# Performance work log

Hardware: AMD Instinct MI355X
Metric: run time of the kernel (lower is better)

The kernel has to match this reference:

```python
import jax, jax.numpy as jnp
import numpy as np

N_TYPES = 4  # global / and / or / leaf node types (indep_weights)


def gcn_layer(x, W_stack, b, edge_src, edge_dst, edge_w, labels, num_nodes):
    # Per-node-type dense projection: compute all 4 projections, then select by label.
    # all4: [4, N, out]
    all4 = jnp.einsum('nd,kdo->kno', x, W_stack)
    support = jnp.take_along_axis(all4, labels[None, :, None].astype(jnp.int32), axis=0)[0]  # [N, out]
    # Sparse adjacency propagation: out[dst] += w * support[src]  (torch.spmm equivalent)
    msgs = support[edge_src] * edge_w[:, None]  # [E, out]
    agg = jax.ops.segment_sum(msgs, edge_dst, num_segments=num_nodes)
    return agg + b


def setup_inputs() -> dict:
    key = jax.random.key(0)
    ks = jax.random.split(key, 12)
    N, E = 50000, 1600000
    nfeat, nhid, nclass = 256, 256, 64
    x = jax.random.normal(ks[0], (N, nfeat), dtype=jnp.float32)
    edge_src = jax.random.randint(ks[1], (E,), 0, N, dtype=jnp.int32)
    edge_dst = jax.random.randint(ks[2], (E,), 0, N, dtype=jnp.int32)
    edge_w = jax.random.uniform(ks[3], (E,), dtype=jnp.float32)
    labels = jax.random.randint(ks[4], (N,), 0, N_TYPES, dtype=jnp.int32)
    def winit(k, fi, fo):
        s = 1.0 / np.sqrt(fo)
        return jax.random.uniform(k, (N_TYPES, fi, fo), minval=-s, maxval=s, dtype=jnp.float32)
    def binit(k, fo):
        s = 1.0 / np.sqrt(fo)
        return jax.random.uniform(k, (fo,), minval=-s, maxval=s, dtype=jnp.float32)
    return {
        'x': x, 'edge_src': edge_src, 'edge_dst': edge_dst, 'edge_w': edge_w, 'labels': labels,
        'W1': winit(ks[5], nfeat, nhid), 'b1': binit(ks[6], nhid),
        'W2': winit(ks[7], nhid, nhid), 'b2': binit(ks[8], nhid),
        'W3': winit(ks[9], nhid, nclass), 'b3': binit(ks[10], nclass),
    }


def reference(x, edge_src, edge_dst, edge_w, labels, W1, b1, W2, b2, W3, b3):
    N = x.shape[0]
    h = jax.nn.relu(gcn_layer(x, W1, b1, edge_src, edge_dst, edge_w, labels, N))
    # F.dropout with p=0 (module default) is identity
    h = jax.nn.relu(gcn_layer(h, W2, b2, edge_src, edge_dst, edge_w, labels, N))
    out = gcn_layer(h, W3, b3, edge_src, edge_dst, edge_w, labels, N)
    return out
```

## Files before the change

### kernel.cpp

```cpp
#include <hip/hip_runtime.h>
#include <hip/hip_bf16.h>

#define NT 4
#define FEAT 256
#define OUT3 64

typedef __bf16 bf16x8 __attribute__((ext_vector_type(8)));
typedef float  f32x4  __attribute__((ext_vector_type(4)));

__device__ inline unsigned int f2bf_bits(float f) {
    __hip_bfloat16 h = __float2bfloat16(f);
    unsigned short u;
    __builtin_memcpy(&u, &h, 2);
    return (unsigned int)u;
}
__device__ inline float bfl(unsigned int u) { return __uint_as_float(u << 16); }
__device__ inline float bfh(unsigned int u) { return __uint_as_float(u & 0xffff0000u); }
__device__ __host__ inline int nat_of(int p) {
    int lo = p & 63;
    return (p & ~63) | (((lo & 3) << 4) | (lo >> 2));
}

__global__ __launch_bounds__(512) void pass_a(const int* __restrict__ dst,
                                              const int* __restrict__ labels,
                                              int* __restrict__ bcnt, int* __restrict__ lc,
                                              int E, int N) {
    __shared__ int h[256];
    __shared__ int lh[NT];
    int tid = threadIdx.x;
    if (tid < 256) h[tid] = 0;
    if (tid < NT) lh[tid] = 0;
    __syncthreads();
    int base = blockIdx.x * 4096;
#pragma unroll
    for (int k = 0; k < 8; ++k) {
        int e = base + k * 512 + tid;
        if (e < E) atomicAdd(&h[((unsigned)dst[e]) >> 8], 1);
    }
#pragma unroll
    for (int k = 0; k < 8; ++k) {
        int i = base + k * 512 + tid;
        if (i < N) atomicAdd(&lh[labels[i]], 1);
    }
    __syncthreads();
    if (tid < 256) { int v = h[tid]; if (v) atomicAdd(&bcnt[tid], v); }
    if (tid < NT) { int v = lh[tid]; if (v) atomicAdd(&lc[tid], v); }
}

__global__ __launch_bounds__(256) void scan_master(
    const int* __restrict__ bcnt, const int* __restrict__ lc,
    int* __restrict__ boff, int* __restrict__ gcur, int* __restrict__ rowoff,
    int* __restrict__ lstart, int NB, int N, int E) {
    __shared__ int s[256];
    int tid = threadIdx.x;
    int own = (tid < NB) ? bcnt[tid] : 0;
    s[tid] = own;
    __syncthreads();
    for (int d = 1; d < 256; d <<= 1) {
        int v = (tid >= d) ? s[tid - d] : 0;
        __syncthreads();
        s[tid] += v;
        __syncthreads();
    }
    int excl = s[tid] - own;
    if (tid < NB) { boff[tid] = excl; gcur[tid] = excl; }
    if (tid == 0) {
        boff[NB] = E; rowoff[N] = E;
        int run = 0;
        for (int l = 0; l < NT; ++l) {
            lstart[l] = run;
            run += (lc[l] + 63) & ~63;
        }
    }
}

__global__ void scatter_nodes(const int* __restrict__ labels, const int* __restrict__ lstart,
                              int* __restrict__ lcur, int* __restrict__ iperm, int N) {
    int n = blockIdx.x * 256 + threadIdx.x;
    int lab = (n < N) ? labels[n] : -1;
    int lane = threadIdx.x & 63;
    for (int l = 0; l < NT; ++l) {
        unsigned long long m = __ballot(lab == l);
        if (m == 0ull) continue;
        int leader = __builtin_ctzll(m);
        int base = 0;
        if (lane == leader) base = atomicAdd(&lcur[l], (int)__popcll(m));
        base = __shfl(base, leader, 64);
        if (lab == l) {
            int prefix = (int)__popcll(m & ((1ull << lane) - 1ull));
            iperm[n] = lstart[l] + base + prefix;
        }
    }
}

__global__ __launch_bounds__(512) void scatter_edges(
    const int* __restrict__ src, const int* __restrict__ dst, const float* __restrict__ w,
    const int* __restrict__ iperm, int* __restrict__ gcur, uint2* __restrict__ earr, int E) {
    __shared__ int h[256];
    __shared__ int basearr[256];
    int tid = threadIdx.x;
    if (tid < 256) h[tid] = 0;
    __syncthreads();
    int base = blockIdx.x * 4096;
    int b[8], rank[8], px[8]; float wv[8];
#pragma unroll
    for (int k = 0; k < 8; ++k) {
        int e = base + k * 512 + tid;
        if (e < E) {
            int d = dst[e];
            b[k] = ((unsigned)d) >> 8;
            px[k] = iperm[src[e]] | ((d & 255) << 16);
            wv[k] = w[e];
            rank[k] = atomicAdd(&h[b[k]], 1);
        } else b[k] = -1;
    }
    __syncthreads();
    if (tid < 256) { int c = h[tid]; basearr[tid] = c ? atomicAdd(&gcur[tid], c) : 0; }
    __syncthreads();
#pragma unroll
    for (int k = 0; k < 8; ++k) {
        if (b[k] >= 0) {
            int pos = basearr[b[k]] + rank[k];
            earr[pos] = make_uint2((unsigned)px[k], __float_as_uint(wv[k]));
        }
    }
}

__global__ __launch_bounds__(1024) void bucket_sort(
    const uint2* __restrict__ earr, const int* __restrict__ boff,
    int* __restrict__ rowoff, unsigned int* __restrict__ edata, int N) {
    int b = blockIdx.x;
    int s = boff[b], e = boff[b + 1];
    __shared__ int cnt[256], off[256];
    int tid = threadIdx.x;
    if (tid < 256) cnt[tid] = 0;
    __syncthreads();
    for (int i = s + tid; i < e; i += 1024) atomicAdd(&cnt[(earr[i].x >> 16) & 255], 1);
    __syncthreads();
    if (tid < 256) off[tid] = cnt[tid];
    __syncthreads();
    for (int d = 1; d < 256; d <<= 1) {
        int v = 0;
        if (tid < 256 && tid >= d) v = off[tid - d];
        __syncthreads();
        if (tid < 256) off[tid] += v;
        __syncthreads();
    }
    if (tid < 256) {
        int excl = off[tid] - cnt[tid];
        int node = b * 256 + tid;
        if (node < N) rowoff[node] = s + excl;
        off[tid] = excl;
    }
    __syncthreads();
    for (int i = s + tid; i < e; i += 1024) {
        uint2 r = earr[i];
        int d = (r.x >> 16) & 255;
        int k = atomicAdd(&off[d], 1);
        edata[s + k] = (f2bf_bits(__uint_as_float(r.y)) << 16) | (r.x & 0xffff);
    }
}

__global__ void cast_x(const float* __restrict__ x, const int* __restrict__ iperm,
                       unsigned short* __restrict__ actLo, unsigned short* __restrict__ actHi,
                       int total4) {
    int i = blockIdx.x * 256 + threadIdx.x;
    if (i < total4) {
        float4 v = ((const float4*)x)[i];
        unsigned int lo = f2bf_bits(v.x) | (f2bf_bits(v.y) << 16);
        unsigned int hi = f2bf_bits(v.z) | (f2bf_bits(v.w) << 16);
        int slot = iperm[i >> 6];
        unsigned short* dst = ((i & 63) >= 32) ? actHi : actLo;
        ((uint2*)dst)[(size_t)slot * 32 + (i & 31)] = make_uint2(lo, hi);
    }
}

__global__ void cast_w_all(const float* __restrict__ W1, const float* __restrict__ W2,
                           const float* __restrict__ W3, const float* __restrict__ b1,
                           const float* __restrict__ b2,
                           unsigned short* __restrict__ W1b, unsigned short* __restrict__ W2b,
                           unsigned short* __restrict__ W3b, float* __restrict__ biasPerm) {
    const int S = NT * FEAT * FEAT;
    const int S3 = NT * FEAT * OUT3;
    int idx = blockIdx.x * 256 + threadIdx.x;
    if (idx < 2 * S + S3) {
        const float* W; unsigned short* D; int OUTF; int t; bool remap;
        if (idx < S)          { W = W1; D = W1b; OUTF = FEAT; t = idx;         remap = false; }
        else if (idx < 2 * S) { W = W2; D = W2b; OUTF = FEAT; t = idx - S;     remap = true; }
        else                  { W = W3; D = W3b; OUTF = OUT3; t = idx - 2 * S; remap = true; }
        int n = t % OUTF;
        int r = t / OUTF;
        int j = r & 7, q = (r >> 3) & 3, k0 = (r >> 5) & 7, lab = r >> 8;
        int k_slot = k0 * 32 + q * 8 + j;
        int k_src = remap ? nat_of(k_slot) : k_slot;
        float f = W[((size_t)(lab * FEAT + k_src)) * OUTF + n];
        D[(((size_t)lab * 8 + k0) * OUTF + n) * 32 + q * 8 + j] = (unsigned short)f2bf_bits(f);
    } else {
        int p = idx - (2 * S + S3);
        if (p < 256) biasPerm[p] = b1[nat_of(p)];
        else if (p < 512) biasPerm[p] = b2[nat_of(p - 256)];
    }
}

__global__ __launch_bounds__(256) void proj256_kernel(
    const unsigned short* __restrict__ actLo, const unsigned short* __restrict__ actHi,
    const unsigned short* __restrict__ Wswz, const int* __restrict__ lstart,
    unsigned short* __restrict__ supLo, unsigned short* __restrict__ supHi) {
    int warp = threadIdx.x >> 6;
    int lane = threadIdx.x & 63;
    int m0 = blockIdx.x * 64;
    int lab = (m0 >= lstart[1]) + (m0 >= lstart[2]) + (m0 >= lstart[3]);
    int q = lane >> 4, c = lane & 15;
    int n0 = warp * 64;

    const unsigned short* aLo = actLo + (size_t)(m0 + c) * 128 + q * 8;
    const unsigned short* aHi = actHi + (size_t)(m0 + c) * 128 + q * 8;
    const unsigned short* bb = Wswz + (size_t)lab * FEAT * 256 + (size_t)(n0 + c) * 32 + q * 8;

    f32x4 acc[4][4] = {};
#pragma unroll
    for (int k0 = 0; k0 < 8; ++k0) {
        const unsigned short* abase = (k0 < 4) ? aLo : aHi;
        int koff = (k0 & 3) * 32;
        bf16x8 a[4];
#pragma unroll
        for (int t = 0; t < 4; ++t) a[t] = *(const bf16x8*)(abase + (size_t)t * 2048 + koff);
        const unsigned short* bk = bb + (size_t)k0 * 32 * 256;
#pragma unroll
        for (int u = 0; u < 4; ++u) {
            bf16x8 bfrag = *(const bf16x8*)(bk + u * 512);
#pragma unroll
            for (int t = 0; t < 4; ++t)
                acc[t][u] = __builtin_amdgcn_mfma_f32_16x16x32_bf16(a[t], bfrag, acc[t][u], 0, 0, 0);
        }
    }
    uint2* ov = (uint2*)((n0 >= 128) ? supHi : supLo);
    int cix = ((n0 & 64) >> 2) + c;
#pragma unroll
    for (int t = 0; t < 4; ++t) {
#pragma unroll
        for (int r = 0; r < 4; ++r) {
            int row = m0 + t * 16 + q * 4 + r;
            unsigned int lo = f2bf_bits(acc[t][0][r]) | (f2bf_bits(acc[t][1][r]) << 16);
            unsigned int hi = f2bf_bits(acc[t][2][r]) | (f2bf_bits(acc[t][3][r]) << 16);
            ov[(size_t)row * 32 + cix] = make_uint2(lo, hi);
        }
    }
}

__global__ __launch_bounds__(256) void proj64_kernel(
    const unsigned short* __restrict__ actLo, const unsigned short* __restrict__ actHi,
    const unsigned short* __restrict__ Wswz, const int* __restrict__ lstart,
    unsigned short* __restrict__ outp) {
    int warp = threadIdx.x >> 6;
    int lane = threadIdx.x & 63;
    int m0 = blockIdx.x * 64;
    int lab = (m0 >= lstart[1]) + (m0 >= lstart[2]) + (m0 >= lstart[3]);
    int q = lane >> 4, c = lane & 15;
    int mb = m0 + warp * 16;

    const unsigned short* aLo = actLo + (size_t)(mb + c) * 128 + q * 8;
    const unsigned short* aHi = actHi + (size_t)(mb + c) * 128 + q * 8;
    const unsigned short* bb = Wswz + (size_t)lab * FEAT * OUT3 + (size_t)c * 32 + q * 8;

    f32x4 acc[4] = {};
#pragma unroll
    for (int k0 = 0; k0 < 8; ++k0) {
        const unsigned short* abase = (k0 < 4) ? aLo : aHi;
        bf16x8 a = *(const bf16x8*)(abase + (k0 & 3) * 32);
        const unsigned short* bk = bb + (size_t)k0 * 32 * OUT3;
#pragma unroll
        for (int u = 0; u < 4; ++u) {
            bf16x8 bfrag = *(const bf16x8*)(bk + u * 512);
            acc[u] = __builtin_amdgcn_mfma_f32_16x16x32_bf16(a, bfrag, acc[u], 0, 0, 0);
        }
    }
    uint2* ov = (uint2*)outp;
#pragma unroll
    for (int r = 0; r < 4; ++r) {
        int row = mb + q * 4 + r;
        unsigned int lo = f2bf_bits(acc[0][r]) | (f2bf_bits(acc[1][r]) << 16);
        unsigned int hi = f2bf_bits(acc[2][r]) | (f2bf_bits(acc[3][r]) << 16);
        ov[(size_t)row * 16 + c] = make_uint2(lo, hi);
    }
}

__global__ __launch_bounds__(256) void agg256h_kernel(
    const unsigned int* __restrict__ sup, const int* __restrict__ rowoff,
    const unsigned int* __restrict__ edata, const int* __restrict__ iperm,
    const float* __restrict__ biasHalf, unsigned int* __restrict__ outp, int N) {
    int warp = __builtin_amdgcn_readfirstlane((int)(threadIdx.x >> 6));
    int node = (int)blockIdx.x * 4 + warp;
    if (node >= N) return;
    int lane = threadIdx.x & 63;
    int s = __builtin_amdgcn_readfirstlane(rowoff[node]);
    int e = __builtin_amdgcn_readfirstlane(rowoff[node + 1]);
    int slot = __builtin_amdgcn_readfirstlane(iperm[node]);
    float a0 = 0.f, a1 = 0.f;
    int j = s;
    for (; j + 16 <= e; j += 16) {
        unsigned int ed[16], v[16];
#pragma unroll
        for (int u = 0; u < 16; ++u) ed[u] = edata[j + u];
#pragma unroll
        for (int u = 0; u < 16; ++u) v[u] = sup[(size_t)(ed[u] & 0xffff) * 64 + lane];
#pragma unroll
        for (int u = 0; u < 16; ++u) {
            float w = __uint_as_float(ed[u] & 0xffff0000u);
            a0 += w * bfl(v[u]); a1 += w * bfh(v[u]);
        }
    }
    if (j < e) {
        unsigned int ed[16], v[16]; float wm[16];
#pragma unroll
        for (int u = 0; u < 16; ++u) {
            int jj = j + u;
            int jc = (jj < e) ? jj : e - 1;
            ed[u] = edata[jc];
            wm[u] = (jj < e) ? __uint_as_float(ed[u] & 0xffff0000u) : 0.f;
        }
#pragma unroll
        for (int u = 0; u < 16; ++u) v[u] = sup[(size_t)(ed[u] & 0xffff) * 64 + lane];
#pragma unroll
        for (int u = 0; u < 16; ++u) { a0 += wm[u] * bfl(v[u]); a1 += wm[u] * bfh(v[u]); }
    }
    float2 b = ((const float2*)biasHalf)[lane];
    a0 = fmaxf(a0 + b.x, 0.f);
    a1 = fmaxf(a1 + b.y, 0.f);
    outp[(size_t)slot * 64 + lane] = f2bf_bits(a0) | (f2bf_bits(a1) << 16);
}

__global__ __launch_bounds__(256) void agg64_kernel(
    const unsigned short* __restrict__ sup, const int* __restrict__ rowoff,
    const unsigned int* __restrict__ edata, const float* __restrict__ b3,
    float* __restrict__ outp, int N) {
    int warp = __builtin_amdgcn_readfirstlane((int)(threadIdx.x >> 6));
    int node = (int)blockIdx.x * 4 + warp;
    if (node >= N) return;
    int lane = threadIdx.x & 63;
    int s = __builtin_amdgcn_readfirstlane(rowoff[node]);
    int e = __builtin_amdgcn_readfirstlane(rowoff[node + 1]);
    float a = 0.f;
    int j = s;
    for (; j + 8 <= e; j += 8) {
        unsigned int ed[8]; unsigned short v[8];
#pragma unroll
        for (int u = 0; u < 8; ++u) ed[u] = edata[j + u];
#pragma unroll
        for (int u = 0; u < 8; ++u) v[u] = sup[(size_t)(ed[u] & 0xffff) * 64 + lane];
#pragma unroll
        for (int u = 0; u < 8; ++u)
            a += __uint_as_float(ed[u] & 0xffff0000u) * __uint_as_float((unsigned int)v[u] << 16);
    }
    if (j < e) {
        unsigned int ed[8]; float wm[8]; unsigned short v[8];
#pragma unroll
        for (int u = 0; u < 8; ++u) {
            int jj = j + u;
            int jc = (jj < e) ? jj : e - 1;
            ed[u] = edata[jc];
            wm[u] = (jj < e) ? __uint_as_float(ed[u] & 0xffff0000u) : 0.f;
        }
#pragma unroll
        for (int u = 0; u < 8; ++u) v[u] = sup[(size_t)(ed[u] & 0xffff) * 64 + lane];
#pragma unroll
        for (int u = 0; u < 8; ++u)
            a += wm[u] * __uint_as_float((unsigned int)v[u] << 16);
    }
    int natp = (((lane & 3) << 4) | (lane >> 2));
    outp[(size_t)node * 64 + natp] = a + b3[natp];
}

extern "C" void kernel_launch(void* const* d_in, const int* in_sizes, int n_in,
                              void* d_out, int out_size, void* d_ws, size_t ws_size,
                              hipStream_t stream) {
    const float* x        = (const float*)d_in[0];
    const int*   edge_src = (const int*)d_in[1];
    const int*   edge_dst = (const int*)d_in[2];
    const float* edge_w   = (const float*)d_in[3];
    const int*   labels   = (const int*)d_in[4];
    const float* W1 = (const float*)d_in[5];
    const float* b1 = (const float*)d_in[6];
    const float* W2 = (const float*)d_in[7];
    const float* b2 = (const float*)d_in[8];
    const float* W3 = (const float*)d_in[9];
    const float* b3 = (const float*)d_in[10];

    const int N = in_sizes[0] / FEAT;
    const int E = in_sizes[1];
    const int NB = (N + 255) >> 8;
    const int G64 = (N + NT * 64 + 63) / 64;
    const int slotCap = G64 * 64;

    char* p = (char*)d_ws;
    auto alloc = [&](size_t bytes) -> char* {
        char* r = p;
        p += (bytes + 255) & ~(size_t)255;
        return r;
    };
    unsigned short* bufA = (unsigned short*)alloc((size_t)slotCap * FEAT * 2);
    unsigned short* bufB = (unsigned short*)alloc((size_t)slotCap * FEAT * 2);
    unsigned short* W1b  = (unsigned short*)alloc((size_t)NT * FEAT * FEAT * 2);
    unsigned short* W2b  = (unsigned short*)alloc((size_t)NT * FEAT * FEAT * 2);
    unsigned short* W3b  = (unsigned short*)alloc((size_t)NT * FEAT * OUT3 * 2);
    float*        biasPerm = (float*)alloc(512 * 4);
    int*          rowoff = (int*)alloc((size_t)(N + 1) * 4);
    unsigned int* edata  = (unsigned int*)alloc((size_t)E * 4);
    int*          iperm  = (int*)alloc((size_t)N * 4);
    int*          counters = (int*)alloc(264 * 4);
    int*          boff   = (int*)alloc(257 * 4);
    int*          gcur   = (int*)alloc(256 * 4);
    int*          lstart = (int*)alloc(64);
    int* bcnt = counters;
    int* lc   = counters + 256;
    int* lcur = counters + 260;

    unsigned short* actLo = bufA;
    unsigned short* actHi = bufA + (size_t)slotCap * 128;
    unsigned short* supLo = bufB;
    unsigned short* supHi = bufB + (size_t)slotCap * 128;
    uint2* earr = (uint2*)bufA;

    const int nbEB = (E + 4095) / 4096;

    hipMemsetAsync(counters, 0, 264 * 4, stream);
    pass_a<<<nbEB, 512, 0, stream>>>(edge_dst, labels, bcnt, lc, E, N);
    scan_master<<<1, 256, 0, stream>>>(bcnt, lc, boff, gcur, rowoff, lstart, NB, N, E);
    scatter_nodes<<<(N + 255) / 256, 256, 0, stream>>>(labels, lstart, lcur, iperm, N);
    scatter_edges<<<nbEB, 512, 0, stream>>>(edge_src, edge_dst, edge_w, iperm, gcur, earr, E);
    bucket_sort<<<NB, 1024, 0, stream>>>(earr, boff, rowoff, edata, N);

    cast_x<<<((N * 64) + 255) / 256, 256, 0, stream>>>(x, iperm, actLo, actHi, N * 64);
    {
        int total = 2 * NT * FEAT * FEAT + NT * FEAT * OUT3 + 512;
        cast_w_all<<<(total + 255) / 256, 256, 0, stream>>>(W1, W2, W3, b1, b2, W1b, W2b, W3b, biasPerm);
    }

    const int aggGrid = (N + 3) / 4;
    proj256_kernel<<<G64, 256, 0, stream>>>(actLo, actHi, W1b, lstart, supLo, supHi);
    agg256h_kernel<<<aggGrid, 256, 0, stream>>>((const unsigned int*)supLo, rowoff, edata, iperm,
                                                biasPerm + 0, (unsigned int*)actLo, N);
    agg256h_kernel<<<aggGrid, 256, 0, stream>>>((const unsigned int*)supHi, rowoff, edata, iperm,
                                                biasPerm + 128, (unsigned int*)actHi, N);
    proj256_kernel<<<G64, 256, 0, stream>>>(actLo, actHi, W2b, lstart, supLo, supHi);
    agg256h_kernel<<<aggGrid, 256, 0, stream>>>((const unsigned int*)supLo, rowoff, edata, iperm,
                                                biasPerm + 256, (unsigned int*)actLo, N);
    agg256h_kernel<<<aggGrid, 256, 0, stream>>>((const unsigned int*)supHi, rowoff, edata, iperm,
                                                biasPerm + 384, (unsigned int*)actHi, N);
    proj64_kernel<<<G64, 256, 0, stream>>>(actLo, actHi, W3b, lstart, bufB);
    agg64_kernel<<<aggGrid, 256, 0, stream>>>(bufB, rowoff, edata, b3, (float*)d_out, N);
}
```

Measured before the change: 501.8 us.

## Merge independent preprocessing kernels into shared launches to overlap work

The edge scatter, x cast and weight cast kernels now run as block ranges of one launch, and the bucket sort runs alongside the first projection GEMM in a second combined launch. The edge staging buffer moves from bufA to the output buffer, so the x cast into bufA no longer conflicts with it. The aim is to cut launch gaps and tail idle time by letting independent stages share the GPU. Bucket sort now uses 256 threads per block instead of 1024, which lengthens each sort block, and the combined kernels may use more registers and reach lower occupancy.

```diff
diff --git a/kernel.cpp b/kernel.cpp
--- a/kernel.cpp
+++ b/kernel.cpp
@@ -93,67 +93,104 @@
     }
 }
 
-__global__ __launch_bounds__(512) void scatter_edges(
+__global__ __launch_bounds__(512) void fuse_a(
     const int* __restrict__ src, const int* __restrict__ dst, const float* __restrict__ w,
-    const int* __restrict__ iperm, int* __restrict__ gcur, uint2* __restrict__ earr, int E) {
-    __shared__ int h[256];
-    __shared__ int basearr[256];
+    const int* __restrict__ iperm, int* __restrict__ gcur, uint2* __restrict__ earr, int E,
+    const float* __restrict__ x, unsigned short* __restrict__ actLo,
+    unsigned short* __restrict__ actHi, int total4,
+    const float* __restrict__ W1, const float* __restrict__ W2, const float* __restrict__ W3,
+    const float* __restrict__ b1, const float* __restrict__ b2,
+    unsigned short* __restrict__ W1b, unsigned short* __restrict__ W2b,
+    unsigned short* __restrict__ W3b, float* __restrict__ biasPerm,
+    int nbEB, int nbX) {
     int tid = threadIdx.x;
-    if (tid < 256) h[tid] = 0;
-    __syncthreads();
-    int base = blockIdx.x * 4096;
-    int b[8], rank[8], px[8]; float wv[8];
-#pragma unroll
-    for (int k = 0; k < 8; ++k) {
-        int e = base + k * 512 + tid;
-        if (e < E) {
-            int d = dst[e];
-            b[k] = ((unsigned)d) >> 8;
-            px[k] = iperm[src[e]] | ((d & 255) << 16);
-            wv[k] = w[e];
-            rank[k] = atomicAdd(&h[b[k]], 1);
-        } else b[k] = -1;
-    }
-    __syncthreads();
-    if (tid < 256) { int c = h[tid]; basearr[tid] = c ? atomicAdd(&gcur[tid], c) : 0; }
-    __syncthreads();
-#pragma unroll
-    for (int k = 0; k < 8; ++k) {
-        if (b[k] >= 0) {
-            int pos = basearr[b[k]] + rank[k];
-            earr[pos] = make_uint2((unsigned)px[k], __float_as_uint(wv[k]));
-        }
-    }
-}
-
-__global__ __launch_bounds__(1024) void bucket_sort(
-    const uint2* __restrict__ earr, const int* __restrict__ boff,
-    int* __restrict__ rowoff, unsigned int* __restrict__ edata, int N) {
-    int b = blockIdx.x;
+    int blk = (int)blockIdx.x;
+    if (blk < nbEB) {
+        __shared__ int h[256];
+        __shared__ int basearr[256];
+        if (tid < 256) h[tid] = 0;
+        __syncthreads();
+        int base = blk * 4096;
+        int b[8], rank[8], px[8]; float wv[8];
+#pragma unroll
+        for (int k = 0; k < 8; ++k) {
+            int e = base + k * 512 + tid;
+            if (e < E) {
+                int d = dst[e];
+                b[k] = ((unsigned)d) >> 8;
+                px[k] = iperm[src[e]] | ((d & 255) << 16);
+                wv[k] = w[e];
+                rank[k] = atomicAdd(&h[b[k]], 1);
+            } else b[k] = -1;
+        }
+        __syncthreads();
+        if (tid < 256) { int c = h[tid]; basearr[tid] = c ? atomicAdd(&gcur[tid], c) : 0; }
+        __syncthreads();
+#pragma unroll
+        for (int k = 0; k < 8; ++k) {
+            if (b[k] >= 0) {
+                int pos = basearr[b[k]] + rank[k];
+                earr[pos] = make_uint2((unsigned)px[k], __float_as_uint(wv[k]));
+            }
+        }
+    } else if (blk < nbEB + nbX) {
+        int i = (blk - nbEB) * 512 + tid;
+        if (i < total4) {
+            float4 v = ((const float4*)x)[i];
+            unsigned int lo = f2bf_bits(v.x) | (f2bf_bits(v.y) << 16);
+            unsigned int hi = f2bf_bits(v.z) | (f2bf_bits(v.w) << 16);
+            int slot = iperm[i >> 6];
+            unsigned short* dp = ((i & 63) >= 32) ? actHi : actLo;
+            ((uint2*)dp)[(size_t)slot * 32 + (i & 31)] = make_uint2(lo, hi);
+        }
+    } else {
+        const int S = NT * FEAT * FEAT;
+        const int S3 = NT * FEAT * OUT3;
+        int idx = (blk - nbEB - nbX) * 512 + tid;
+        if (idx < 2 * S + S3) {
+            const float* W; unsigned short* D; int OUTF; int t; bool remap;
+            if (idx < S)          { W = W1; D = W1b; OUTF = FEAT; t = idx;         remap = false; }
+            else if (idx < 2 * S) { W = W2; D = W2b; OUTF = FEAT; t = idx - S;     remap = true; }
+            else                  { W = W3; D = W3b; OUTF = OUT3; t = idx - 2 * S; remap = true; }
+            int n = t % OUTF;
+            int r = t / OUTF;
+            int j = r & 7, q = (r >> 3) & 3, k0 = (r >> 5) & 7, lab = r >> 8;
+            int k_slot = k0 * 32 + q * 8 + j;
+            int k_src = remap ? nat_of(k_slot) : k_slot;
+            float f = W[((size_t)(lab * FEAT + k_src)) * OUTF + n];
+            D[(((size_t)lab * 8 + k0) * OUTF + n) * 32 + q * 8 + j] = (unsigned short)f2bf_bits(f);
+        } else {
+            int p2 = idx - (2 * S + S3);
+            if (p2 < 256) biasPerm[p2] = b1[nat_of(p2)];
+            else if (p2 < 512) biasPerm[p2] = b2[nat_of(p2 - 256)];
+        }
+    }
+}
+
+__device__ void bucket_sort_body(int b, const uint2* __restrict__ earr,
+                                 const int* __restrict__ boff, int* __restrict__ rowoff,
+                                 unsigned int* __restrict__ edata, int N) {
     int s = boff[b], e = boff[b + 1];
     __shared__ int cnt[256], off[256];
     int tid = threadIdx.x;
-    if (tid < 256) cnt[tid] = 0;
-    __syncthreads();
-    for (int i = s + tid; i < e; i += 1024) atomicAdd(&cnt[(earr[i].x >> 16) & 255], 1);
-    __syncthreads();
-    if (tid < 256) off[tid] = cnt[tid];
+    cnt[tid] = 0;
+    __syncthreads();
+    for (int i = s + tid; i < e; i += 256) atomicAdd(&cnt[(earr[i].x >> 16) & 255], 1);
+    __syncthreads();
+    off[tid] = cnt[tid];
     __syncthreads();
     for (int d = 1; d < 256; d <<= 1) {
-        int v = 0;
-        if (tid < 256 && tid >= d) v = off[tid - d];
-        __syncthreads();
-        if (tid < 256) off[tid] += v;
-        __syncthreads();
-    }
-    if (tid < 256) {
-        int excl = off[tid] - cnt[tid];
-        int node = b * 256 + tid;
-        if (node < N) rowoff[node] = s + excl;
-        off[tid] = excl;
-    }
-    __syncthreads();
-    for (int i = s + tid; i < e; i += 1024) {
+        int v = (tid >= d) ? off[tid - d] : 0;
+        __syncthreads();
+        off[tid] += v;
+        __syncthreads();
+    }
+    int excl = off[tid] - cnt[tid];
+    int node = b * 256 + tid;
+    if (node < N) rowoff[node] = s + excl;
+    off[tid] = excl;
+    __syncthreads();
+    for (int i = s + tid; i < e; i += 256) {
         uint2 r = earr[i];
         int d = (r.x >> 16) & 255;
         int k = atomicAdd(&off[d], 1);
@@ -161,54 +198,16 @@
     }
 }
 
-__global__ void cast_x(const float* __restrict__ x, const int* __restrict__ iperm,
-                       unsigned short* __restrict__ actLo, unsigned short* __restrict__ actHi,
-                       int total4) {
-    int i = blockIdx.x * 256 + threadIdx.x;
-    if (i < total4) {
-        float4 v = ((const float4*)x)[i];
-        unsigned int lo = f2bf_bits(v.x) | (f2bf_bits(v.y) << 16);
-        unsigned int hi = f2bf_bits(v.z) | (f2bf_bits(v.w) << 16);
-        int slot = iperm[i >> 6];
-        unsigned short* dst = ((i & 63) >= 32) ? actHi : actLo;
-        ((uint2*)dst)[(size_t)slot * 32 + (i & 31)] = make_uint2(lo, hi);
-    }
-}
-
-__global__ void cast_w_all(const float* __restrict__ W1, const float* __restrict__ W2,
-                           const float* __restrict__ W3, const float* __restrict__ b1,
-                           const float* __restrict__ b2,
-                           unsigned short* __restrict__ W1b, unsigned short* __restrict__ W2b,
-                           unsigned short* __restrict__ W3b, float* __restrict__ biasPerm) {
-    const int S = NT * FEAT * FEAT;
-    const int S3 = NT * FEAT * OUT3;
-    int idx = blockIdx.x * 256 + threadIdx.x;
-    if (idx < 2 * S + S3) {
-        const float* W; unsigned short* D; int OUTF; int t; bool remap;
-        if (idx < S)          { W = W1; D = W1b; OUTF = FEAT; t = idx;         remap = false; }
-        else if (idx < 2 * S) { W = W2; D = W2b; OUTF = FEAT; t = idx - S;     remap = true; }
-        else                  { W = W3; D = W3b; OUTF = OUT3; t = idx - 2 * S; remap = true; }
-        int n = t % OUTF;
-        int r = t / OUTF;
-        int j = r & 7, q = (r >> 3) & 3, k0 = (r >> 5) & 7, lab = r >> 8;
-        int k_slot = k0 * 32 + q * 8 + j;
-        int k_src = remap ? nat_of(k_slot) : k_slot;
-        float f = W[((size_t)(lab * FEAT + k_src)) * OUTF + n];
-        D[(((size_t)lab * 8 + k0) * OUTF + n) * 32 + q * 8 + j] = (unsigned short)f2bf_bits(f);
-    } else {
-        int p = idx - (2 * S + S3);
-        if (p < 256) biasPerm[p] = b1[nat_of(p)];
-        else if (p < 512) biasPerm[p] = b2[nat_of(p - 256)];
-    }
-}
-
-__global__ __launch_bounds__(256) void proj256_kernel(
-    const unsigned short* __restrict__ actLo, const unsigned short* __restrict__ actHi,
-    const unsigned short* __restrict__ Wswz, const int* __restrict__ lstart,
-    unsigned short* __restrict__ supLo, unsigned short* __restrict__ supHi) {
+__device__ void proj256_body(int gb,
+                             const unsigned short* __restrict__ actLo,
+                             const unsigned short* __restrict__ actHi,
+                             const unsigned short* __restrict__ Wswz,
+                             const int* __restrict__ lstart,
+                             unsigned short* __restrict__ supLo,
+                             unsigned short* __restrict__ supHi) {
     int warp = threadIdx.x >> 6;
     int lane = threadIdx.x & 63;
-    int m0 = blockIdx.x * 64;
+    int m0 = gb * 64;
     int lab = (m0 >= lstart[1]) + (m0 >= lstart[2]) + (m0 >= lstart[3]);
     int q = lane >> 4, c = lane & 15;
     int n0 = warp * 64;
@@ -246,6 +245,24 @@
             ov[(size_t)row * 32 + cix] = make_uint2(lo, hi);
         }
     }
+}
+
+__global__ __launch_bounds__(256) void fuse_b(
+    const uint2* __restrict__ earr, const int* __restrict__ boff,
+    int* __restrict__ rowoff, unsigned int* __restrict__ edata, int N, int NB,
+    const unsigned short* __restrict__ actLo, const unsigned short* __restrict__ actHi,
+    const unsigned short* __restrict__ Wswz, const int* __restrict__ lstart,
+    unsigned short* __restrict__ supLo, unsigned short* __restrict__ supHi) {
+    int blk = (int)blockIdx.x;
+    if (blk < NB) bucket_sort_body(blk, earr, boff, rowoff, edata, N);
+    else proj256_body(blk - NB, actLo, actHi, Wswz, lstart, supLo, supHi);
+}
+
+__global__ __launch_bounds__(256) void proj256_kernel(
+    const unsigned short* __restrict__ actLo, const unsigned short* __restrict__ actHi,
+    const unsigned short* __restrict__ Wswz, const int* __restrict__ lstart,
+    unsigned short* __restrict__ supLo, unsigned short* __restrict__ supHi) {
+    proj256_body((int)blockIdx.x, actLo, actHi, Wswz, lstart, supLo, supHi);
 }
 
 __global__ __launch_bounds__(256) void proj64_kernel(
@@ -419,25 +436,26 @@
     unsigned short* actHi = bufA + (size_t)slotCap * 128;
     unsigned short* supLo = bufB;
     unsigned short* supHi = bufB + (size_t)slotCap * 128;
-    uint2* earr = (uint2*)bufA;
+    uint2* earr = (uint2*)d_out;
 
     const int nbEB = (E + 4095) / 4096;
+    const int total4 = N * 64;
+    const int nbX = (total4 + 511) / 512;
+    const int totW = 2 * NT * FEAT * FEAT + NT * FEAT * OUT3 + 512;
+    const int nbW = (totW + 511) / 512;
 
     hipMemsetAsync(counters, 0, 264 * 4, stream);
     pass_a<<<nbEB, 512, 0, stream>>>(edge_dst, labels, bcnt, lc, E, N);
     scan_master<<<1, 256, 0, stream>>>(bcnt, lc, boff, gcur, rowoff, lstart, NB, N, E);
     scatter_nodes<<<(N + 255) / 256, 256, 0, stream>>>(labels, lstart, lcur, iperm, N);
-    scatter_edges<<<nbEB, 512, 0, stream>>>(edge_src, edge_dst, edge_w, iperm, gcur, earr, E);
-    bucket_sort<<<NB, 1024, 0, stream>>>(earr, boff, rowoff, edata, N);
-
-    cast_x<<<((N * 64) + 255) / 256, 256, 0, stream>>>(x, iperm, actLo, actHi, N * 64);
-    {
-        int total = 2 * NT * FEAT * FEAT + NT * FEAT * OUT3 + 512;
-        cast_w_all<<<(total + 255) / 256, 256, 0, stream>>>(W1, W2, W3, b1, b2, W1b, W2b, W3b, biasPerm);
-    }
+    fuse_a<<<nbEB + nbX + nbW, 512, 0, stream>>>(
+        edge_src, edge_dst, edge_w, iperm, gcur, earr, E,
+        x, actLo, actHi, total4,
+        W1, W2, W3, b1, b2, W1b, W2b, W3b, biasPerm, nbEB, nbX);
 
     const int aggGrid = (N + 3) / 4;
-    proj256_kernel<<<G64, 256, 0, stream>>>(actLo, actHi, W1b, lstart, supLo, supHi);
+    fuse_b<<<NB + G64, 256, 0, stream>>>(earr, boff, rowoff, edata, N, NB,
+                                         actLo, actHi, W1b, lstart, supLo, supHi);
     agg256h_kernel<<<aggGrid, 256, 0, stream>>>((const unsigned int*)supLo, rowoff, edata, iperm,
                                                 biasPerm + 0, (unsigned int*)actLo, N);
     agg256h_kernel<<<aggGrid, 256, 0, stream>>>((const unsigned int*)supHi, rowoff, edata, iperm,
```

After: 482.3 us. 1.04x faster.
